# Optimization experiments

Hardware: AMD Instinct MI355X
Metric: run time of the kernel (lower is better)

The kernel has to match this reference:

```python
import jax, jax.numpy as jnp
import numpy as np

N = 50000
D = 128
E = 600000


def setup_inputs() -> dict:
    key = jax.random.key(0)
    k1, k2, k3, k4, k5, k6 = jax.random.split(key, 6)
    x = jax.random.normal(k1, (N, D), dtype=jnp.float32)
    edge_index = jax.random.randint(k2, (2, E), 0, N, dtype=jnp.int32)
    s = 1.0 / np.sqrt(D)
    W1 = jax.random.uniform(k3, (D, D), dtype=jnp.float32, minval=-s, maxval=s)
    b1 = jax.random.uniform(k4, (D,), dtype=jnp.float32, minval=-s, maxval=s)
    W2 = jax.random.uniform(k5, (D, D), dtype=jnp.float32, minval=-s, maxval=s)
    b2 = jax.random.uniform(k6, (D,), dtype=jnp.float32, minval=-s, maxval=s)
    return {"x": x, "edge_index": edge_index, "W1": W1, "b1": b1, "W2": W2, "b2": b2}


def _gcn_conv(x, src, dst, W, b):
    # PyG GCNConv (default flow source->target): out[dst] += norm * (x @ W)[src] + b
    n = x.shape[0]
    deg = jax.ops.segment_sum(jnp.ones_like(dst, dtype=x.dtype), dst, num_segments=n)
    dinv = jnp.where(deg > 0, jax.lax.rsqrt(deg), 0.0)
    norm = dinv[src] * dinv[dst]          # [E+N]
    h = x @ W                             # [N, D]
    msg = h[src] * norm[:, None]          # [E+N, D] gather + scale
    out = jax.ops.segment_sum(msg, dst, num_segments=n)
    return out + b


def reference(x, edge_index, W1, b1, W2, b2):
    n = x.shape[0]
    loops = jnp.arange(n, dtype=edge_index.dtype)
    src = jnp.concatenate([edge_index[0], loops])  # add self-loops
    dst = jnp.concatenate([edge_index[1], loops])
    h = jax.nn.relu(_gcn_conv(x, src, dst, W1, b1))
    out = jax.nn.relu(_gcn_conv(h, src, dst, W2, b2))
    return out
```

## Files before the change

kernel.cpp:

```cpp
#include <hip/hip_runtime.h>
#include <stdint.h>

typedef __attribute__((ext_vector_type(8))) short bf16x8;
typedef __attribute__((ext_vector_type(4))) float f32x4;

#define CAP 64

__device__ __forceinline__ float bf2f(unsigned int u) {
    union { unsigned int i; float f; } v; v.i = u << 16; return v.f;
}
__device__ __forceinline__ unsigned int f2bf(float f) {
    union { float f; unsigned int i; } v; v.f = f;
    unsigned int b = v.i;
    b += 0x7FFFu + ((b >> 16) & 1u);
    return b >> 16;
}


__global__ void bucket_kernel(const int* __restrict__ src, const int* __restrict__ dst,
                              int* __restrict__ counts, unsigned short* __restrict__ bucket,
                              int E,
                              const float* __restrict__ W1, const float* __restrict__ W2,
                              unsigned short* __restrict__ Wt1, unsigned short* __restrict__ Wt2) {
    int t = blockIdx.x * 256 + threadIdx.x;
    if (t < 32768) {
        const float* W = (t < 16384) ? W1 : W2;
        unsigned short* O = (t < 16384) ? Wt1 : Wt2;
        int i = t & 16383;
        O[i] = (unsigned short)f2bf(W[(i & 127) * 128 + (i >> 7)]);
    }
    if (t < E) {
        int s = src[t], d = dst[t];
        int slot = atomicAdd(&counts[d], 1);
        if (slot < CAP) bucket[(size_t)d * CAP + slot] = (unsigned short)s;
    }
}


template <bool A_BF16>
__global__ __launch_bounds__(256) void gemm128(const void* __restrict__ Av,
                                               const unsigned short* __restrict__ Wt,
                                               const int* __restrict__ counts,
                                               unsigned short* __restrict__ G, int M) {
    int t = threadIdx.x;
    int wave = t >> 6, lane = t & 63;
    int m0 = (blockIdx.x * 4 + wave) * 16;
    int mrow = lane & 15, quad = lane >> 4;

    int arow = m0 + mrow;
    int srow = arow < M ? arow : M - 1;

    f32x4 acc[8];
#pragma unroll
    for (int nt = 0; nt < 8; ++nt) acc[nt] = (f32x4){0.f, 0.f, 0.f, 0.f};

#pragma unroll
    for (int kb = 0; kb < 4; ++kb) {
        bf16x8 a;
        if (A_BF16) {
            const unsigned short* Arow = (const unsigned short*)Av + (size_t)srow * 128;
            a = *(const bf16x8*)(Arow + kb * 32 + quad * 8);
        } else {
            const float* Arow = (const float*)Av + (size_t)srow * 128;
            f32x4 lo = *(const f32x4*)(Arow + kb * 32 + quad * 8);
            f32x4 hi = *(const f32x4*)(Arow + kb * 32 + quad * 8 + 4);
#pragma unroll
            for (int i = 0; i < 4; ++i) { a[i] = (short)f2bf(lo[i]); a[i + 4] = (short)f2bf(hi[i]); }
        }
#pragma unroll
        for (int nt = 0; nt < 8; ++nt) {
            bf16x8 b = *(const bf16x8*)(Wt + (size_t)(nt * 16 + mrow) * 128 + kb * 32 + quad * 8);
            acc[nt] = __builtin_amdgcn_mfma_f32_16x16x32_bf16(a, b, acc[nt], 0, 0, 0);
        }
    }

#pragma unroll
    for (int r = 0; r < 4; ++r) {
        int row = m0 + quad * 4 + r;
        if (row < M) {
            float dr = rsqrtf((float)counts[row] + 1.0f);
#pragma unroll
            for (int nt = 0; nt < 8; ++nt)
                G[(size_t)row * 128 + nt * 16 + mrow] = (unsigned short)f2bf(acc[nt][r] * dr);
        }
    }
}


template <bool OUT_BF16>
__global__ __launch_bounds__(256) void agg_kernel(const unsigned short* __restrict__ g,
                                                  const int* __restrict__ counts,
                                                  const unsigned short* __restrict__ bucket,
                                                  const float* __restrict__ bias,
                                                  void* __restrict__ out, int N) {
    int lane = threadIdx.x & 63;
    int n = blockIdx.x * 4 + (threadIdx.x >> 6);
    if (n >= N) return;

    const unsigned int* g32 = (const unsigned int*)g;
    int deg = counts[n];
    int m = min(deg, CAP);
    float di = rsqrtf((float)deg + 1.0f);
    int sv = bucket[(size_t)n * CAP + lane];

    unsigned int hv = g32[(size_t)n * 64 + lane];
    float a0 = bf2f(hv & 0xFFFFu);
    float a1 = bf2f(hv >> 16);
    float c0 = 0.f, c1 = 0.f;

#pragma unroll 1
    for (int j0 = 0; j0 < m; j0 += 16) {
        const unsigned int* rp[16];
        float w[16];
#pragma unroll
        for (int u = 0; u < 16; ++u) {
            int idx = j0 + u;
            int cid = idx < m ? idx : m - 1;
            int s = __builtin_amdgcn_readlane(sv, cid);
            rp[u] = g32 + (size_t)s * 64;
            w[u] = idx < m ? 1.f : 0.f;
        }
        unsigned int v[16];
#pragma unroll
        for (int u = 0; u < 16; ++u) v[u] = rp[u][lane];
#pragma unroll
        for (int u = 0; u < 16; ++u) {
            if (u & 1) {
                c0 = fmaf(w[u], bf2f(v[u] & 0xFFFFu), c0);
                c1 = fmaf(w[u], bf2f(v[u] >> 16), c1);
            } else {
                a0 = fmaf(w[u], bf2f(v[u] & 0xFFFFu), a0);
                a1 = fmaf(w[u], bf2f(v[u] >> 16), a1);
            }
        }
    }

    float2 bv = ((const float2*)bias)[lane];
    float o0 = fmaxf((a0 + c0) * di + bv.x, 0.f);
    float o1 = fmaxf((a1 + c1) * di + bv.y, 0.f);
    if (OUT_BF16) {
        ((unsigned int*)out)[(size_t)n * 64 + lane] = f2bf(o0) | (f2bf(o1) << 16);
    } else {
        ((float2*)out)[(size_t)n * 64 + lane] = make_float2(o0, o1);
    }
}


extern "C" void kernel_launch(void* const* d_in, const int* in_sizes, int n_in,
                              void* d_out, int out_size, void* d_ws, size_t ws_size,
                              hipStream_t stream) {
    const float* x  = (const float*)d_in[0];
    const int*   ei = (const int*)d_in[1];
    const float* W1 = (const float*)d_in[2];
    const float* b1 = (const float*)d_in[3];
    const float* W2 = (const float*)d_in[4];
    const float* b2 = (const float*)d_in[5];
    float* out = (float*)d_out;

    int N = in_sizes[0] / 128;
    int E = in_sizes[1] / 2;
    const int* src = ei;
    const int* dst = ei + E;

    char* p = (char*)d_ws;
    auto alloc = [&](size_t bytes) {
        char* r = p; p += (bytes + 255) & ~(size_t)255; return r;
    };
    int*            counts = (int*)           alloc((size_t)N * 4);
    unsigned short* bucket = (unsigned short*)alloc((size_t)N * CAP * 2);
    unsigned short* g1     = (unsigned short*)alloc((size_t)N * 128 * 2);
    unsigned short* out1   = (unsigned short*)alloc((size_t)N * 128 * 2);
    unsigned short* Wt1    = (unsigned short*)alloc(16384 * 2);
    unsigned short* Wt2    = (unsigned short*)alloc(16384 * 2);

    hipMemsetAsync(counts, 0, (size_t)N * 4, stream);
    bucket_kernel<<<(E + 255) / 256, 256, 0, stream>>>(src, dst, counts, bucket, E,
                                                       W1, W2, Wt1, Wt2);

    int gblocks = (N + 63) / 64;
    gemm128<false><<<gblocks, 256, 0, stream>>>(x, Wt1, counts, g1, N);
    agg_kernel<true><<<(N + 3) / 4, 256, 0, stream>>>(g1, counts, bucket, b1, out1, N);
    gemm128<true><<<gblocks, 256, 0, stream>>>(out1, Wt2, counts, g1, N);
    agg_kernel<false><<<(N + 3) / 4, 256, 0, stream>>>(g1, counts, bucket, b2, out, N);
}
```

Before: 213.3 us.

## Fuse layer-1 aggregation with layer-2 GEMM via shared-memory staging

Layer-1 neighbor aggregation and the layer-2 dense transform now run in one kernel. Each block aggregates 16 nodes (4 per wave), writes the bf16 activations to LDS, and then does a 16x128x128 MFMA GEMM with the 128 output columns split across the 4 waves. This removes one kernel launch and the global write and read of the intermediate activation. The cost is that each wave now walks 4 nodes one after another, giving less memory parallelism per wave, and the GEMM tile is small.

After: 195.8 us, median of 2. -8.2%, faster.

```diff
diff --git a/kernel.cpp b/kernel.cpp
--- a/kernel.cpp
+++ b/kernel.cpp
@@ -37,8 +37,7 @@
 }
 
 
-template <bool A_BF16>
-__global__ __launch_bounds__(256) void gemm128(const void* __restrict__ Av,
+__global__ __launch_bounds__(256) void gemm128(const float* __restrict__ A,
                                                const unsigned short* __restrict__ Wt,
                                                const int* __restrict__ counts,
                                                unsigned short* __restrict__ G, int M) {
@@ -49,6 +48,7 @@
 
     int arow = m0 + mrow;
     int srow = arow < M ? arow : M - 1;
+    const float* Arow = A + (size_t)srow * 128;
 
     f32x4 acc[8];
 #pragma unroll
@@ -56,17 +56,11 @@
 
 #pragma unroll
     for (int kb = 0; kb < 4; ++kb) {
+        f32x4 lo = *(const f32x4*)(Arow + kb * 32 + quad * 8);
+        f32x4 hi = *(const f32x4*)(Arow + kb * 32 + quad * 8 + 4);
         bf16x8 a;
-        if (A_BF16) {
-            const unsigned short* Arow = (const unsigned short*)Av + (size_t)srow * 128;
-            a = *(const bf16x8*)(Arow + kb * 32 + quad * 8);
-        } else {
-            const float* Arow = (const float*)Av + (size_t)srow * 128;
-            f32x4 lo = *(const f32x4*)(Arow + kb * 32 + quad * 8);
-            f32x4 hi = *(const f32x4*)(Arow + kb * 32 + quad * 8 + 4);
-#pragma unroll
-            for (int i = 0; i < 4; ++i) { a[i] = (short)f2bf(lo[i]); a[i + 4] = (short)f2bf(hi[i]); }
-        }
+#pragma unroll
+        for (int i = 0; i < 4; ++i) { a[i] = (short)f2bf(lo[i]); a[i + 4] = (short)f2bf(hi[i]); }
 #pragma unroll
         for (int nt = 0; nt < 8; ++nt) {
             bf16x8 b = *(const bf16x8*)(Wt + (size_t)(nt * 16 + mrow) * 128 + kb * 32 + quad * 8);
@@ -87,12 +81,100 @@
 }
 
 
-template <bool OUT_BF16>
-__global__ __launch_bounds__(256) void agg_kernel(const unsigned short* __restrict__ g,
-                                                  const int* __restrict__ counts,
-                                                  const unsigned short* __restrict__ bucket,
-                                                  const float* __restrict__ bias,
-                                                  void* __restrict__ out, int N) {
+__global__ __launch_bounds__(256) void fused_agg_gemm(const unsigned short* __restrict__ g,
+                                                      const int* __restrict__ counts,
+                                                      const unsigned short* __restrict__ bucket,
+                                                      const float* __restrict__ bias,
+                                                      const unsigned short* __restrict__ Wt,
+                                                      unsigned short* __restrict__ G2, int N) {
+    __shared__ __align__(16) unsigned short As[16][136];
+    int wave = threadIdx.x >> 6, lane = threadIdx.x & 63;
+    const unsigned int* g32 = (const unsigned int*)g;
+    int nb0 = blockIdx.x * 16 + wave * 4;
+
+    int degs[4]; int svs[4]; unsigned int hvs[4];
+#pragma unroll
+    for (int i = 0; i < 4; ++i) {
+        int n = min(nb0 + i, N - 1);
+        degs[i] = counts[n];
+        svs[i]  = bucket[(size_t)n * CAP + lane];
+        hvs[i]  = g32[(size_t)n * 64 + lane];
+    }
+    float2 bv = ((const float2*)bias)[lane];
+
+#pragma unroll 1
+    for (int i = 0; i < 4; ++i) {
+        int m = min(degs[i], CAP);
+        float di = rsqrtf((float)degs[i] + 1.0f);
+        float a0 = bf2f(hvs[i] & 0xFFFFu);
+        float a1 = bf2f(hvs[i] >> 16);
+        float c0 = 0.f, c1 = 0.f;
+#pragma unroll 1
+        for (int j0 = 0; j0 < m; j0 += 16) {
+            const unsigned int* rp[16];
+            float w[16];
+#pragma unroll
+            for (int u = 0; u < 16; ++u) {
+                int idx = j0 + u;
+                int cid = idx < m ? idx : m - 1;
+                int s = __builtin_amdgcn_readlane(svs[i], cid);
+                rp[u] = g32 + (size_t)s * 64;
+                w[u] = idx < m ? 1.f : 0.f;
+            }
+            unsigned int v[16];
+#pragma unroll
+            for (int u = 0; u < 16; ++u) v[u] = rp[u][lane];
+#pragma unroll
+            for (int u = 0; u < 16; ++u) {
+                if (u & 1) {
+                    c0 = fmaf(w[u], bf2f(v[u] & 0xFFFFu), c0);
+                    c1 = fmaf(w[u], bf2f(v[u] >> 16), c1);
+                } else {
+                    a0 = fmaf(w[u], bf2f(v[u] & 0xFFFFu), a0);
+                    a1 = fmaf(w[u], bf2f(v[u] >> 16), a1);
+                }
+            }
+        }
+        float o0 = fmaxf((a0 + c0) * di + bv.x, 0.f);
+        float o1 = fmaxf((a1 + c1) * di + bv.y, 0.f);
+        *(unsigned int*)&As[wave * 4 + i][lane * 2] = f2bf(o0) | (f2bf(o1) << 16);
+    }
+    __syncthreads();
+
+    int mrow = lane & 15, quad = lane >> 4;
+    f32x4 acc[2];
+    acc[0] = (f32x4){0.f, 0.f, 0.f, 0.f};
+    acc[1] = (f32x4){0.f, 0.f, 0.f, 0.f};
+#pragma unroll
+    for (int kb = 0; kb < 4; ++kb) {
+        bf16x8 a = *(const bf16x8*)(&As[mrow][kb * 32 + quad * 8]);
+#pragma unroll
+        for (int q = 0; q < 2; ++q) {
+            int nt = wave * 2 + q;
+            bf16x8 b = *(const bf16x8*)(Wt + (size_t)(nt * 16 + mrow) * 128 + kb * 32 + quad * 8);
+            acc[q] = __builtin_amdgcn_mfma_f32_16x16x32_bf16(a, b, acc[q], 0, 0, 0);
+        }
+    }
+#pragma unroll
+    for (int r = 0; r < 4; ++r) {
+        int row = blockIdx.x * 16 + quad * 4 + r;
+        if (row < N) {
+            float dr = rsqrtf((float)counts[row] + 1.0f);
+#pragma unroll
+            for (int q = 0; q < 2; ++q) {
+                int nt = wave * 2 + q;
+                G2[(size_t)row * 128 + nt * 16 + mrow] = (unsigned short)f2bf(acc[q][r] * dr);
+            }
+        }
+    }
+}
+
+
+__global__ __launch_bounds__(256) void agg_final(const unsigned short* __restrict__ g,
+                                                 const int* __restrict__ counts,
+                                                 const unsigned short* __restrict__ bucket,
+                                                 const float* __restrict__ bias,
+                                                 float* __restrict__ out, int N) {
     int lane = threadIdx.x & 63;
     int n = blockIdx.x * 4 + (threadIdx.x >> 6);
     if (n >= N) return;
@@ -138,11 +220,7 @@
     float2 bv = ((const float2*)bias)[lane];
     float o0 = fmaxf((a0 + c0) * di + bv.x, 0.f);
     float o1 = fmaxf((a1 + c1) * di + bv.y, 0.f);
-    if (OUT_BF16) {
-        ((unsigned int*)out)[(size_t)n * 64 + lane] = f2bf(o0) | (f2bf(o1) << 16);
-    } else {
-        ((float2*)out)[(size_t)n * 64 + lane] = make_float2(o0, o1);
-    }
+    ((float2*)out)[(size_t)n * 64 + lane] = make_float2(o0, o1);
 }
 
 
@@ -169,7 +247,7 @@
     int*            counts = (int*)           alloc((size_t)N * 4);
     unsigned short* bucket = (unsigned short*)alloc((size_t)N * CAP * 2);
     unsigned short* g1     = (unsigned short*)alloc((size_t)N * 128 * 2);
-    unsigned short* out1   = (unsigned short*)alloc((size_t)N * 128 * 2);
+    unsigned short* g2     = (unsigned short*)alloc((size_t)N * 128 * 2);
     unsigned short* Wt1    = (unsigned short*)alloc(16384 * 2);
     unsigned short* Wt2    = (unsigned short*)alloc(16384 * 2);
 
@@ -177,9 +255,7 @@
     bucket_kernel<<<(E + 255) / 256, 256, 0, stream>>>(src, dst, counts, bucket, E,
                                                        W1, W2, Wt1, Wt2);
 
-    int gblocks = (N + 63) / 64;
-    gemm128<false><<<gblocks, 256, 0, stream>>>(x, Wt1, counts, g1, N);
-    agg_kernel<true><<<(N + 3) / 4, 256, 0, stream>>>(g1, counts, bucket, b1, out1, N);
-    gemm128<true><<<gblocks, 256, 0, stream>>>(out1, Wt2, counts, g1, N);
-    agg_kernel<false><<<(N + 3) / 4, 256, 0, stream>>>(g1, counts, bucket, b2, out, N);
-}
+    gemm128<<<(N + 63) / 64, 256, 0, stream>>>(x, Wt1, counts, g1, N);
+    fused_agg_gemm<<<(N + 15) / 16, 256, 0, stream>>>(g1, counts, bucket, b1, Wt2, g2, N);
+    agg_final<<<(N + 3) / 4, 256, 0, stream>>>(g2, counts, bucket, b2, out, N);
+}
```
